# Performance work log

Measured on AMD Instinct MI355X. Metric: run time of the kernel, lower is better.

Reference implementation:

```python
import jax, jax.numpy as jnp
import numpy as np
from jax import lax

H_HEADS = 8      # attention heads
C_HID = 32       # per-head channels
NEG_SLOPE = 0.2  # PyG GATConv default leaky_relu slope


def _gat(x, src, dst, W, a_src, a_dst, b, num_nodes):
    # x: (N, Din); src/dst: (E',) with self-loops already appended
    h = (x @ W).reshape(num_nodes, H_HEADS, C_HID)          # (N, H, C)
    e = jax.nn.leaky_relu((h * a_src).sum(-1)[src] + (h * a_dst).sum(-1)[dst], NEG_SLOPE)  # (E', H)
    emax = jax.ops.segment_max(e, dst, num_segments=num_nodes)
    ex = jnp.exp(e - emax[dst])
    denom = jax.ops.segment_sum(ex, dst, num_segments=num_nodes)
    alpha = ex / (denom[dst] + 1e-16)                        # segment softmax over incoming edges
    out = jax.ops.segment_sum(h[src] * alpha[:, :, None], dst, num_segments=num_nodes)
    return out.reshape(num_nodes, H_HEADS * C_HID) + b


def _lstm_dir(seq, Wih, Whh, bih, bhh):
    # seq: (K, D); single-direction LSTM, returns final hidden state (Hs,)
    Hs = Whh.shape[1]
    def step(carry, x):
        h, c = carry
        g = x @ Wih.T + h @ Whh.T + bih + bhh                # (4*Hs,)
        i, f, gg, o = jnp.split(g, 4)
        c = jax.nn.sigmoid(f) * c + jax.nn.sigmoid(i) * jnp.tanh(gg)
        h = jax.nn.sigmoid(o) * jnp.tanh(c)
        return (h, c), None
    (h, _), _ = lax.scan(step, (jnp.zeros(Hs, seq.dtype), jnp.zeros(Hs, seq.dtype)), seq)
    return h


def setup_inputs():
    key = jax.random.key(0)
    ks = jax.random.split(key, 20)
    K, N, E = 8, 10000, 160000
    D1, D2, LH = 1, H_HEADS * C_HID, 256   # D2 = 256
    s = 0.1
    inp = {}
    inp['xs'] = jax.random.normal(ks[0], (K, N, D1), jnp.float32)
    inp['edge_index'] = jax.random.randint(ks[1], (K, 2, E), 0, N, jnp.int32)
    inp['W1'] = jax.random.normal(ks[2], (D1, D2), jnp.float32) * s
    inp['a_src1'] = jax.random.normal(ks[3], (H_HEADS, C_HID), jnp.float32) * s
    inp['a_dst1'] = jax.random.normal(ks[4], (H_HEADS, C_HID), jnp.float32) * s
    inp['b1'] = jnp.zeros((D2,), jnp.float32)
    inp['W2'] = jax.random.normal(ks[5], (D2, D2), jnp.float32) * s
    inp['a_src2'] = jax.random.normal(ks[6], (H_HEADS, C_HID), jnp.float32) * s
    inp['a_dst2'] = jax.random.normal(ks[7], (H_HEADS, C_HID), jnp.float32) * s
    inp['b2'] = jnp.zeros((D2,), jnp.float32)
    inp['Wih_f'] = jax.random.normal(ks[8], (4 * LH, D2), jnp.float32) * s
    inp['Whh_f'] = jax.random.normal(ks[9], (4 * LH, LH), jnp.float32) * s
    inp['bih_f'] = jnp.zeros((4 * LH,), jnp.float32)
    inp['bhh_f'] = jnp.zeros((4 * LH,), jnp.float32)
    inp['Wih_b'] = jax.random.normal(ks[10], (4 * LH, D2), jnp.float32) * s
    inp['Whh_b'] = jax.random.normal(ks[11], (4 * LH, LH), jnp.float32) * s
    inp['bih_b'] = jnp.zeros((4 * LH,), jnp.float32)
    inp['bhh_b'] = jnp.zeros((4 * LH,), jnp.float32)
    return inp


def reference(xs, edge_index, W1, a_src1, a_dst1, b1, W2, a_src2, a_dst2, b2,
              Wih_f, Whh_f, bih_f, bhh_f, Wih_b, Whh_b, bih_b, bhh_b):
    N = xs.shape[1]
    loops = jnp.arange(N, dtype=edge_index.dtype)  # self-loops (PyG default)
    def snap(carry, inp):
        x, ei = inp
        src = jnp.concatenate([ei[0], loops])
        dst = jnp.concatenate([ei[1], loops])
        h = jax.nn.relu(_gat(x, src, dst, W1, a_src1, a_dst1, b1, N))
        h = jax.nn.relu(_gat(h, src, dst, W2, a_src2, a_dst2, b2, N))
        return carry, h.mean(0)   # global mean pool -> (256,)
    _, embs = lax.scan(snap, 0, (xs, edge_index))   # (K, 256)
    h_fwd = _lstm_dir(embs, Wih_f, Whh_f, bih_f, bhh_f)
    h_bwd = _lstm_dir(embs[::-1], Wih_b, Whh_b, bih_b, bhh_b)
    return jnp.concatenate([h_fwd, h_bwd])[None, :]  # (1, 512)
```

## Files before the change

### kernel.cpp

```cpp
#include <hip/hip_runtime.h>
#include <hip/hip_fp16.h>
#include <math.h>

#define H_HEADS 8
#define C_HID 32
#define D2 256
#define NEG_SLOPE 0.2f
#define KSTEPS 8

__device__ __forceinline__ float lrelu(float x) { return x < 0.f ? NEG_SLOPE * x : x; }
__device__ __forceinline__ float sigmoidf(float x) { return 1.f / (1.f + expf(-x)); }


__global__ void zero_all_kernel(int* counts, int* fill, double* embp, int KN, int NEMBP,
                                const float* __restrict__ W1, const float* __restrict__ a_src1,
                                const float* __restrict__ a_dst1, float* Pvec, int D1) {
    int tid = blockIdx.x * blockDim.x + threadIdx.x;
    if (tid < KN) { counts[tid] = 0; fill[tid] = 0; }
    if (tid < NEMBP) embp[tid] = 0.0;
    if (blockIdx.x == 0 && threadIdx.x < 16 && D1 == 1) {
        int h = threadIdx.x & 7;
        const float* a = (threadIdx.x >= 8) ? a_dst1 : a_src1;
        float s = 0.f;
        for (int c = 0; c < 32; ++c) s += W1[h * 32 + c] * a[h * 32 + c];
        Pvec[threadIdx.x] = s;
    }
}


__global__ void count_all_kernel(const int* __restrict__ ei, int E, int N, int K,
                                 int* __restrict__ counts) {
    int bid = blockIdx.x;
    int k = bid % K;
    int jb = bid / K;
    int j = jb * blockDim.x + threadIdx.x;
    if (j >= E + N) return;
    int d = (j < E) ? ei[(size_t)k * 2 * E + E + j] : (j - E);
    atomicAdd(&counts[(size_t)k * N + d], 1);
}

__global__ __launch_bounds__(1024) void scan_all_kernel(const int* __restrict__ counts,
                                                        int* __restrict__ row_ptr, int N) {
    int k = blockIdx.x;
    const int* cnt = counts + (size_t)k * N;
    int* rp = row_ptr + (size_t)k * (N + 1);
    __shared__ int part[1024];
    int t = threadIdx.x;
    int ipt = (N + 1023) >> 10;
    int begin = t * ipt;
    int end = begin + ipt; if (end > N) end = N;
    if (begin > N) begin = N;
    int s = 0;
    for (int i = begin; i < end; ++i) s += cnt[i];
    part[t] = s;
    __syncthreads();
    for (int d = 1; d < 1024; d <<= 1) {
        int v = 0;
        if (t >= d) v = part[t - d];
        __syncthreads();
        if (t >= d) part[t] += v;
        __syncthreads();
    }
    int run = (t == 0) ? 0 : part[t - 1];
    for (int i = begin; i < end; ++i) { rp[i] = run; run += cnt[i]; }
    if (t == 1023) rp[N] = part[1023];
}

__global__ void scatter_all_kernel(const int* __restrict__ ei, int E, int N, int K,
                                   const int* __restrict__ row_ptr, int* __restrict__ fill,
                                   int* __restrict__ ein) {
    int bid = blockIdx.x;
    int k = bid % K;
    int jb = bid / K;
    int j = jb * blockDim.x + threadIdx.x;
    if (j >= E + N) return;
    int s, d;
    if (j < E) { s = ei[(size_t)k * 2 * E + j]; d = ei[(size_t)k * 2 * E + E + j]; }
    else { s = j - E; d = s; }
    int pos = row_ptr[(size_t)k * (N + 1) + d] + atomicAdd(&fill[(size_t)k * N + d], 1);
    ein[(size_t)k * (E + N) + pos] = s;
}


__global__ __launch_bounds__(256) void agg1s_all_kernel(const float* __restrict__ xs,
                                                        const float* __restrict__ P,
                                                        const int* __restrict__ row_ptr,
                                                        const int* __restrict__ ein,
                                                        float* __restrict__ Sbuf,
                                                        int N, int E2, int k0, int BKcur) {
    int bid = blockIdx.x;
    int kb = bid % BKcur;
    int nb = bid / BKcur;
    int k = k0 + kb;
    const float* x = xs + (size_t)k * N;
    const int* rp = row_ptr + (size_t)k * (N + 1);
    const int* ek = ein + (size_t)k * E2;

    int n = nb * 4 + (threadIdx.x >> 6);
    if (n >= N) return;
    int lane = threadIdx.x & 63;
    int e0 = rp[n], e1 = rp[n + 1];
    int h8 = lane & 7;
    float Ps = P[h8], Pd = P[8 + h8];
    float base = x[n] * Pd;

    float mx = -INFINITY;
    for (int i = e0 + (lane >> 3); i < e1; i += 8) {
        float xv = x[ek[i]];
        mx = fmaxf(mx, lrelu(xv * Ps + base));
    }
    mx = fmaxf(mx, __shfl_xor(mx, 8));
    mx = fmaxf(mx, __shfl_xor(mx, 16));
    mx = fmaxf(mx, __shfl_xor(mx, 32));

    float num = 0.f, den = 0.f;
    for (int i = e0 + (lane >> 3); i < e1; i += 8) {
        float xv = x[ek[i]];
        float w = __expf(lrelu(xv * Ps + base) - mx);
        num += w * xv;
        den += w;
    }
    num += __shfl_xor(num, 8);  den += __shfl_xor(den, 8);
    num += __shfl_xor(num, 16); den += __shfl_xor(den, 16);
    num += __shfl_xor(num, 32); den += __shfl_xor(den, 32);
    float S = num / (den + 1e-16f);

    if (lane < 8) Sbuf[((size_t)kb * N + n) * 8 + lane] = S;
}


__global__ void h1_kernel(const float* __restrict__ x, const float* __restrict__ W,
                          float* __restrict__ h, int N, int D1) {
    int tid = blockIdx.x * blockDim.x + threadIdx.x;
    if (tid >= N * 256) return;
    int n = tid >> 8, j = tid & 255;
    float acc = 0.f;
    for (int d = 0; d < D1; ++d) acc += x[n * D1 + d] * W[d * 256 + j];
    h[tid] = acc;
}

__global__ __launch_bounds__(256) void s_all_kernel(const float* __restrict__ bufA,
                                                    const float* __restrict__ a_src,
                                                    const float* __restrict__ a_dst,
                                                    float* __restrict__ s_src,
                                                    float* __restrict__ s_dst, int N) {
    int kb = blockIdx.y;
    int j = blockIdx.x * 256 + threadIdx.x;
    if (j >= N * 8) return;
    int n = j >> 3, hh = j & 7;
    const float* hp = bufA + (size_t)kb * N * 256 + (size_t)n * 256 + hh * 32;
    const float* as = a_src + hh * 32;
    const float* ad = a_dst + hh * 32;
    float ss = 0.f, sd = 0.f;
#pragma unroll
    for (int c = 0; c < 32; ++c) { float v = hp[c]; ss += v * as[c]; sd += v * ad[c]; }
    s_src[(size_t)kb * N * 8 + j] = ss;
    s_dst[(size_t)kb * N * 8 + j] = sd;
}

__global__ __launch_bounds__(256) void s_all_h16_kernel(const __half* __restrict__ h16,
                                                        const float* __restrict__ a_src,
                                                        const float* __restrict__ a_dst,
                                                        float* __restrict__ s_src,
                                                        float* __restrict__ s_dst, int N) {
    int kb = blockIdx.y;
    int j = blockIdx.x * 256 + threadIdx.x;
    if (j >= N * 8) return;
    int n = j >> 3, hh = j & 7;
    const __half2* hp = (const __half2*)(h16 + (size_t)kb * N * 256 + (size_t)n * 256 + hh * 32);
    const float* as = a_src + hh * 32;
    const float* ad = a_dst + hh * 32;
    float ss = 0.f, sd = 0.f;
#pragma unroll
    for (int c = 0; c < 16; ++c) {
        float2 v = __half22float2(hp[c]);
        ss += v.x * as[2 * c] + v.y * as[2 * c + 1];
        sd += v.x * ad[2 * c] + v.y * ad[2 * c + 1];
    }
    s_src[(size_t)kb * N * 8 + j] = ss;
    s_dst[(size_t)kb * N * 8 + j] = sd;
}

__global__ __launch_bounds__(256) void agg2_out_kernel(const float* __restrict__ h,
                                                       const float* __restrict__ s_src,
                                                       const float* __restrict__ s_dst,
                                                       const int* __restrict__ row_ptr,
                                                       const int* __restrict__ ein,
                                                       const float* __restrict__ bias,
                                                       float* __restrict__ out,
                                                       int N, int E2, int k0) {
    int k = k0;
    const int* rp = row_ptr + (size_t)k * (N + 1);
    const int* ek = ein + (size_t)k * E2;
    int n = blockIdx.x * 4 + (threadIdx.x >> 6);
    if (n >= N) return;
    int lane = threadIdx.x & 63;
    int e0 = rp[n], e1 = rp[n + 1];
    int h8 = lane & 7;
    float sd8 = s_dst[n * 8 + h8];

    float mx = -INFINITY;
    for (int i = e0 + (lane >> 3); i < e1; i += 8) {
        int s = ek[i];
        mx = fmaxf(mx, lrelu(s_src[s * 8 + h8] + sd8));
    }
    mx = fmaxf(mx, __shfl_xor(mx, 8));
    mx = fmaxf(mx, __shfl_xor(mx, 16));
    mx = fmaxf(mx, __shfl_xor(mx, 32));

    int hd = lane >> 3;
    float m = __shfl(mx, hd);
    float sdh = __shfl(sd8, hd);

    float den = 0.f;
    float4 acc = make_float4(0.f, 0.f, 0.f, 0.f);
    for (int i = e0; i < e1; ++i) {
        int s = ek[i];
        const float4 hv = *(const float4*)(h + (size_t)s * 256 + lane * 4);
        float w = expf(lrelu(s_src[s * 8 + hd] + sdh) - m);
        den += w;
        acc.x += w * hv.x; acc.y += w * hv.y; acc.z += w * hv.z; acc.w += w * hv.w;
    }
    float dE = den + 1e-16f;
    const float4 bv = *(const float4*)(bias + lane * 4);
    float4 o;
    o.x = fmaxf(acc.x / dE + bv.x, 0.f);
    o.y = fmaxf(acc.y / dE + bv.y, 0.f);
    o.z = fmaxf(acc.z / dE + bv.z, 0.f);
    o.w = fmaxf(acc.w / dE + bv.w, 0.f);
    *(float4*)(out + (size_t)n * 256 + lane * 4) = o;
}

__global__ void cvt_kernel(const float* __restrict__ src, __half* __restrict__ dst, int total) {
    int i = blockIdx.x * blockDim.x + threadIdx.x;
    if (i * 2 + 1 < total) {
        float2 v = *(const float2*)(src + i * 2);
        ((__half2*)dst)[i] = __floats2half2_rn(v.x, v.y);
    }
}


__global__ __launch_bounds__(256) void agg2pool_kernel(const __half* __restrict__ h16,
                                                       const float* __restrict__ s_src,
                                                       const float* __restrict__ s_dst,
                                                       const int* __restrict__ row_ptr,
                                                       const int* __restrict__ ein,
                                                       const float* __restrict__ bias,
                                                       double* __restrict__ embp,
                                                       int N, int E2, int k0, int BKcur) {
    int bid = blockIdx.x;
    int kb = bid % BKcur;
    int nb = bid / BKcur;
    int k = k0 + kb;
    int w = threadIdx.x >> 6;
    int lane = threadIdx.x & 63;
    int n = nb * 4 + w;
    bool active = (n < N);
    const __half* h = h16 + (size_t)kb * N * 256;
    const float* ssrc = s_src + (size_t)kb * N * 8;
    const float* sdst = s_dst + (size_t)kb * N * 8;
    const int* rp = row_ptr + (size_t)k * (N + 1);
    const int* ek = ein + (size_t)k * E2;

    float4 o = make_float4(0.f, 0.f, 0.f, 0.f);
    if (active) {
        int e0 = rp[n], e1 = rp[n + 1];
        int h8 = lane & 7;
        int es = lane >> 3;
        int hd = lane >> 3;
        float sd8 = sdst[n * 8 + h8];

        float mx = -INFINITY;
        for (int i = e0 + es; i < e1; i += 8) {
            int s = ek[i];
            mx = fmaxf(mx, lrelu(ssrc[s * 8 + h8] + sd8));
        }
        mx = fmaxf(mx, __shfl_xor(mx, 8));
        mx = fmaxf(mx, __shfl_xor(mx, 16));
        mx = fmaxf(mx, __shfl_xor(mx, 32));

        float den = 0.f;
        float4 acc = make_float4(0.f, 0.f, 0.f, 0.f);

        for (int c0 = e0; c0 < e1; c0 += 8) {
            int eI = c0 + es;
            bool valid = (eI < e1);
            int sA = ek[valid ? eI : e0];
            float wv = __expf(lrelu(ssrc[sA * 8 + h8] + sd8) - mx);
            if (!valid) wv = 0.f;

            int jmax = e1 - c0; if (jmax > 8) jmax = 8;
#pragma unroll 8
            for (int j = 0; j < 8; ++j) {
                if (j >= jmax) break;
                int srcLane = (j << 3) + hd;
                float wj = __shfl(wv, srcLane);
                int sj = __shfl(sA, srcLane);
                const __half2* hp = (const __half2*)(h + (size_t)sj * 256 + lane * 4);
                float2 f0 = __half22float2(hp[0]);
                float2 f1 = __half22float2(hp[1]);
                den += wj;
                acc.x += wj * f0.x;
                acc.y += wj * f0.y;
                acc.z += wj * f1.x;
                acc.w += wj * f1.y;
            }
        }
        float dE = den + 1e-16f;
        const float4 bv = *(const float4*)(bias + lane * 4);
        o.x = fmaxf(acc.x / dE + bv.x, 0.f);
        o.y = fmaxf(acc.y / dE + bv.y, 0.f);
        o.z = fmaxf(acc.z / dE + bv.z, 0.f);
        o.w = fmaxf(acc.w / dE + bv.w, 0.f);
    }

    __shared__ double pe[4][256];
    pe[w][lane * 4 + 0] = (double)o.x;
    pe[w][lane * 4 + 1] = (double)o.y;
    pe[w][lane * 4 + 2] = (double)o.z;
    pe[w][lane * 4 + 3] = (double)o.w;
    __syncthreads();
    int tid = threadIdx.x;
    double s = pe[0][tid] + pe[1][tid] + pe[2][tid] + pe[3][tid];
    atomicAdd(&embp[((size_t)k * 32 + (nb & 31)) * 256 + tid], s);
}


__global__ __launch_bounds__(256) void gemm_fused_kernel(const float* __restrict__ S,
                                                         const float* __restrict__ W1,
                                                         const float* __restrict__ bias1,
                                                         const float* __restrict__ B,
                                                         __half* __restrict__ C16, int M) {
    __shared__ float Ast[16][132];
    __shared__ float Bs[16][132];
    __shared__ float w1s[256], b1s[256];
    __shared__ float Ss[128 * 8];
    int tid = threadIdx.x;
    int bm = blockIdx.x, bn = blockIdx.y;

    w1s[tid] = W1[tid];
    b1s[tid] = bias1[tid];
    {
        int base = bm * 128 * 8 + tid * 4;
        float4 sv = make_float4(0.f, 0.f, 0.f, 0.f);
        if (bm * 128 + (tid * 4) / 8 < M) {
            sv = *(const float4*)(S + base);
        }
        *(float4*)&Ss[tid * 4] = sv;
    }

    int arow = tid >> 1;
    int kgrp = (tid & 1) * 8;
    bool rowvalid = (bm * 128 + arow < M);

    int brow = tid >> 4;
    int bcol = (tid & 15) * 8;
    const float* Bbase = B + bn * 128;

    int w = tid >> 6, lane = tid & 63;
    int qr = (w >> 1) * 64, qc = (w & 1) * 64;
    int ty = lane >> 3, tx = lane & 7;
    int r0 = qr + ty * 8, c0 = qc + tx * 8;
    float acc[8][8] = {};

    __syncthreads();

    for (int kt = 0; kt < 256; kt += 16) {
        float sh = Ss[arow * 8 + (kt >> 5)];
#pragma unroll
        for (int j = 0; j < 8; ++j) {
            int kk = kgrp + j;
            float a = fmaxf(fmaf(sh, w1s[kt + kk], b1s[kt + kk]), 0.f);
            Ast[kk][arow] = rowvalid ? a : 0.f;
        }
        const float* bg = Bbase + (size_t)(kt + brow) * 256 + bcol;
        *(float4*)&Bs[brow][bcol] = *(const float4*)bg;
        *(float4*)&Bs[brow][bcol + 4] = *(const float4*)(bg + 4);
        __syncthreads();
#pragma unroll
        for (int kk = 0; kk < 16; ++kk) {
            float4 a0 = *(const float4*)&Ast[kk][r0];
            float4 a1 = *(const float4*)&Ast[kk][r0 + 4];
            float4 b0 = *(const float4*)&Bs[kk][c0];
            float4 b1v = *(const float4*)&Bs[kk][c0 + 4];
            float ar[8] = {a0.x, a0.y, a0.z, a0.w, a1.x, a1.y, a1.z, a1.w};
            float br[8] = {b0.x, b0.y, b0.z, b0.w, b1v.x, b1v.y, b1v.z, b1v.w};
#pragma unroll
            for (int i2 = 0; i2 < 8; ++i2)
#pragma unroll
                for (int j2 = 0; j2 < 8; ++j2) acc[i2][j2] += ar[i2] * br[j2];
        }
        __syncthreads();
    }
#pragma unroll
    for (int i2 = 0; i2 < 8; ++i2) {
        int gm = bm * 128 + r0 + i2;
        if (gm < M) {
            float4 pack;
            ((__half2*)&pack)[0] = __floats2half2_rn(acc[i2][0], acc[i2][1]);
            ((__half2*)&pack)[1] = __floats2half2_rn(acc[i2][2], acc[i2][3]);
            ((__half2*)&pack)[2] = __floats2half2_rn(acc[i2][4], acc[i2][5]);
            ((__half2*)&pack)[3] = __floats2half2_rn(acc[i2][6], acc[i2][7]);
            *(float4*)(C16 + (size_t)gm * 256 + bn * 128 + c0) = pack;
        }
    }
}


__global__ __launch_bounds__(256) void gemm_kernel(const float* __restrict__ A,
                                                   const float* __restrict__ B,
                                                   float* __restrict__ C, int M) {
    __shared__ float Ast[8][132];
    __shared__ float Bs[8][128];
    int tid = threadIdx.x;
    int bm = blockIdx.x, bn = blockIdx.y;
    int ty = tid >> 4, tx = tid & 15;
    int r0 = ty * 8, c0 = tx * 8;
    float acc[8][8] = {};
    int arow = tid >> 1, acol = (tid & 1) * 4;
    int brow = tid >> 5, bcol = (tid & 31) * 4;
    const float* Bbase = B + bn * 128;

    for (int kt = 0; kt < 256; kt += 8) {
        int gr = bm * 128 + arow;
        float4 av = (gr < M) ? *(const float4*)(A + (size_t)gr * 256 + kt + acol)
                             : make_float4(0.f, 0.f, 0.f, 0.f);
        Ast[acol + 0][arow] = av.x;
        Ast[acol + 1][arow] = av.y;
        Ast[acol + 2][arow] = av.z;
        Ast[acol + 3][arow] = av.w;
        *(float4*)&Bs[brow][bcol] = *(const float4*)(Bbase + (size_t)(kt + brow) * 256 + bcol);
        __syncthreads();
#pragma unroll
        for (int kk = 0; kk < 8; ++kk) {
            float4 a0 = *(const float4*)&Ast[kk][r0];
            float4 a1 = *(const float4*)&Ast[kk][r0 + 4];
            float4 b0 = *(const float4*)&Bs[kk][c0];
            float4 b1 = *(const float4*)&Bs[kk][c0 + 4];
            float ar[8] = {a0.x, a0.y, a0.z, a0.w, a1.x, a1.y, a1.z, a1.w};
            float br[8] = {b0.x, b0.y, b0.z, b0.w, b1.x, b1.y, b1.z, b1.w};
#pragma unroll
            for (int i2 = 0; i2 < 8; ++i2)
#pragma unroll
                for (int j2 = 0; j2 < 8; ++j2) acc[i2][j2] += ar[i2] * br[j2];
        }
        __syncthreads();
    }
#pragma unroll
    for (int i2 = 0; i2 < 8; ++i2) {
        int gm = bm * 128 + r0 + i2;
        if (gm < M) {
            *(float4*)(C + (size_t)gm * 256 + bn * 128 + c0) =
                make_float4(acc[i2][0], acc[i2][1], acc[i2][2], acc[i2][3]);
            *(float4*)(C + (size_t)gm * 256 + bn * 128 + c0 + 4) =
                make_float4(acc[i2][4], acc[i2][5], acc[i2][6], acc[i2][7]);
        }
    }
}


__global__ void merge_kernel(const double* __restrict__ embp, float* __restrict__ emb,
                             int* __restrict__ flags) {
    int k = blockIdx.x, c = threadIdx.x;
    double s = 0.0;
#pragma unroll
    for (int p = 0; p < 32; ++p) s += embp[((size_t)k * 32 + p) * 256 + c];
    emb[k * 256 + c] = (float)s;
    if (blockIdx.x == 0 && threadIdx.x < 2 * (KSTEPS + 1)) flags[threadIdx.x] = 0;
}


__global__ __launch_bounds__(256) void lstm_rec_kernel(
    const float* __restrict__ emb, float invN,
    const float* __restrict__ Wih_f, const float* __restrict__ Whh_f,
    const float* __restrict__ bih_f, const float* __restrict__ bhh_f,
    const float* __restrict__ Wih_b, const float* __restrict__ Whh_b,
    const float* __restrict__ bih_b, const float* __restrict__ bhh_b,
    float* __restrict__ hbuf, int* __restrict__ flags, float* __restrict__ out) {
    int dir = blockIdx.x >> 4;
    int seg = blockIdx.x & 15;
    const float* Wih = dir ? Wih_b : Wih_f;
    const float* Whh = dir ? Whh_b : Whh_f;
    const float* bih = dir ? bih_b : bih_f;
    const float* bhh = dir ? bhh_b : bhh_f;

    __shared__ float wh[64 * 256];
    __shared__ float wi[64 * 256];
    __shared__ float xs_s[KSTEPS * 256];
    __shared__ float gx[KSTEPS][64];
    __shared__ float garr[64];
    __shared__ float hprev_s[256];
    int tid = threadIdx.x;

    for (int v = tid; v < 64 * 64; v += 256) {
        int lrow = v >> 6;
        int c4 = (v & 63) * 4;
        int grow = ((lrow >> 4) << 8) + seg * 16 + (lrow & 15);
        *(float4*)&wh[lrow * 256 + c4] = *(const float4*)(Whh + (size_t)grow * 256 + c4);
        *(float4*)&wi[lrow * 256 + c4] = *(const float4*)(Wih + (size_t)grow * 256 + c4);
    }
    for (int idx = tid; idx < KSTEPS * 256; idx += 256) xs_s[idx] = emb[idx] * invN;
    __syncthreads();

    for (int d = tid; d < KSTEPS * 64; d += 256) {
        int st = d >> 6, lr = d & 63;
        const float* wr = &wi[lr << 8];
        const float* xr = &xs_s[st << 8];
        int r = (tid & 63) << 2;
        float acc = 0.f;
#pragma unroll 8
        for (int kk = 0; kk < 256; kk += 4) {
            int k2 = (kk + r) & 255;
            acc += wr[k2] * xr[k2] + wr[k2 + 1] * xr[k2 + 1] +
                   wr[k2 + 2] * xr[k2 + 2] + wr[k2 + 3] * xr[k2 + 3];
        }
        int grow = ((lr >> 4) << 8) + seg * 16 + (lr & 15);
        gx[st][lr] = acc + bih[grow] + bhh[grow];
    }

    int* flag = flags + dir * (KSTEPS + 1);
    float* hb = hbuf + dir * (KSTEPS + 1) * 256;

    if (tid < 16)
        __hip_atomic_store(&hb[seg * 16 + tid], 0.f, __ATOMIC_RELAXED, __HIP_MEMORY_SCOPE_AGENT);
    __syncthreads();
    if (tid == 0)
        __hip_atomic_fetch_add(&flag[0], 1, __ATOMIC_RELEASE, __HIP_MEMORY_SCOPE_AGENT);

    float c_reg = 0.f;

    for (int step = 0; step < KSTEPS; ++step) {
        if (tid == 0) {
            while (__hip_atomic_load(&flag[step], __ATOMIC_RELAXED, __HIP_MEMORY_SCOPE_AGENT) < 16) {
                __builtin_amdgcn_s_sleep(1);
            }
            (void)__hip_atomic_load(&flag[step], __ATOMIC_ACQUIRE, __HIP_MEMORY_SCOPE_AGENT);
        }
        __syncthreads();
        hprev_s[tid] = __hip_atomic_load(&hb[step * 256 + tid], __ATOMIC_RELAXED,
                                         __HIP_MEMORY_SCOPE_AGENT);
        __syncthreads();

        int d = tid >> 2, p = tid & 3;
        const float* wr = &wh[(d << 8) + (p << 6)];
        const float* hr = &hprev_s[p << 6];
        int rot = tid & 63;
        float acc = 0.f;
#pragma unroll 8
        for (int k = 0; k < 64; ++k) {
            int k2 = (k + rot) & 63;
            acc += wr[k2] * hr[k2];
        }
        acc += __shfl_xor(acc, 1);
        acc += __shfl_xor(acc, 2);
        if (p == 0) garr[d] = acc;
        __syncthreads();

        if (tid < 16) {
            float ig = sigmoidf(garr[tid] + gx[step][tid]);
            float fg = sigmoidf(garr[16 + tid] + gx[step][16 + tid]);
            float gg = tanhf(garr[32 + tid] + gx[step][32 + tid]);
            float og = sigmoidf(garr[48 + tid] + gx[step][48 + tid]);
            float cn = fg * c_reg + ig * gg;
            c_reg = cn;
            float hn = og * tanhf(cn);
            __hip_atomic_store(&hb[(step + 1) * 256 + seg * 16 + tid], hn, __ATOMIC_RELAXED,
                               __HIP_MEMORY_SCOPE_AGENT);
        }
        __syncthreads();
        if (tid == 0)
            __hip_atomic_fetch_add(&flag[step + 1], 1, __ATOMIC_RELEASE, __HIP_MEMORY_SCOPE_AGENT);
    }

    if (tid < 16)
        out[dir * 256 + seg * 16 + tid] =
            __hip_atomic_load(&hb[KSTEPS * 256 + seg * 16 + tid], __ATOMIC_RELAXED,
                              __HIP_MEMORY_SCOPE_AGENT);
}


extern "C" void kernel_launch(void* const* d_in, const int* in_sizes, int n_in,
                              void* d_out, int out_size, void* d_ws, size_t ws_size,
                              hipStream_t stream) {
    const float* xs = (const float*)d_in[0];
    const int* edge_index = (const int*)d_in[1];
    const float* W1 = (const float*)d_in[2];
    const float* a_src1 = (const float*)d_in[3];
    const float* a_dst1 = (const float*)d_in[4];
    const float* b1 = (const float*)d_in[5];
    const float* W2 = (const float*)d_in[6];
    const float* a_src2 = (const float*)d_in[7];
    const float* a_dst2 = (const float*)d_in[8];
    const float* b2 = (const float*)d_in[9];
    const float* Wih_f = (const float*)d_in[10];
    const float* Whh_f = (const float*)d_in[11];
    const float* bih_f = (const float*)d_in[12];
    const float* bhh_f = (const float*)d_in[13];
    const float* Wih_b = (const float*)d_in[14];
    const float* Whh_b = (const float*)d_in[15];
    const float* bih_b = (const float*)d_in[16];
    const float* bhh_b = (const float*)d_in[17];

    const int K = KSTEPS;
    int D1 = in_sizes[2] / D2;
    int N = in_sizes[0] / (K * D1);
    int E = in_sizes[1] / (2 * K);
    int E2 = E + N;

    auto al = [](size_t x) { return (x + 255) & ~(size_t)255; };
    size_t fixed_sz = al((size_t)K * N * 4)
                    + al((size_t)K * (N + 1) * 4)
                    + al((size_t)K * N * 4)
                    + al((size_t)K * E2 * 4)
                    + al((size_t)K * 32 * 256 * 8)
                    + al((size_t)K * 256 * 4)
                    + al((size_t)2 * (K + 1) * 256 * 4)
                    + al((size_t)2 * (K + 1) * 4)
                    + al(16 * 4);
    int BK = 8;
    while (BK > 1) {
        size_t need = fixed_sz + 3 * al((size_t)BK * N * 8 * 4) + 2 * al((size_t)BK * N * 256 * 4);
        if (need <= ws_size) break;
        BK >>= 1;
    }

    char* w = (char*)d_ws;
    auto alloc = [&](size_t bytes) { char* p = w; w += (bytes + 255) & ~(size_t)255; return p; };
    int* counts = (int*)alloc((size_t)K * N * 4);
    int* row_ptr = (int*)alloc((size_t)K * (N + 1) * 4);
    int* fill = (int*)alloc((size_t)K * N * 4);
    int* ein = (int*)alloc((size_t)K * E2 * 4);
    double* embp = (double*)alloc((size_t)K * 32 * 256 * 8);
    float* emb = (float*)alloc((size_t)K * 256 * 4);
    float* hbuf = (float*)alloc((size_t)2 * (K + 1) * 256 * 4);
    int* flags = (int*)alloc((size_t)2 * (K + 1) * 4);
    float* Pvec = (float*)alloc(16 * 4);
    float* Sbuf = (float*)alloc((size_t)BK * N * 8 * 4);
    float* s_src = (float*)alloc((size_t)BK * N * 8 * 4);
    float* s_dst = (float*)alloc((size_t)BK * N * 8 * 4);
    float* bufA = (float*)alloc((size_t)BK * N * 256 * 4);
    float* bufB = (float*)alloc((size_t)BK * N * 256 * 4);
    __half* h16 = (__half*)bufA;
    __half* h16_fb = (__half*)bufB;

    int KN = K * N;
    int NEMBP = K * 32 * 256;
    int zblk = ((KN > NEMBP ? KN : NEMBP) + 255) / 256;
    zero_all_kernel<<<zblk, 256, 0, stream>>>(counts, fill, embp, KN, NEMBP,
                                              W1, a_src1, a_dst1, Pvec, D1);
    int eblk = (E2 + 255) / 256;
    count_all_kernel<<<eblk * K, 256, 0, stream>>>(edge_index, E, N, K, counts);
    scan_all_kernel<<<K, 1024, 0, stream>>>(counts, row_ptr, N);
    scatter_all_kernel<<<eblk * K, 256, 0, stream>>>(edge_index, E, N, K, row_ptr, fill, ein);

    int nblk4 = (N + 3) / 4;
    int sblk = (N * 8 + 255) / 256;
    for (int k0 = 0; k0 < K; k0 += BK) {
        int BKcur = (K - k0 < BK) ? (K - k0) : BK;
        if (D1 == 1) {
            agg1s_all_kernel<<<nblk4 * BKcur, 256, 0, stream>>>(
                xs, Pvec, row_ptr, ein, Sbuf, N, E2, k0, BKcur);
            int M = BKcur * N;
            gemm_fused_kernel<<<dim3((M + 127) / 128, 2), 256, 0, stream>>>(
                Sbuf, W1, b1, W2, h16, M);
            s_all_h16_kernel<<<dim3(sblk, BKcur), 256, 0, stream>>>(h16, a_src2, a_dst2,
                                                                    s_src, s_dst, N);
            agg2pool_kernel<<<nblk4 * BKcur, 256, 0, stream>>>(
                h16, s_src, s_dst, row_ptr, ein, b2, embp, N, E2, k0, BKcur);
        } else {
            for (int kk = 0; kk < BKcur; ++kk) {
                int k = k0 + kk;
                const float* xk = xs + (size_t)k * N * D1;
                h1_kernel<<<(N * 256 + 255) / 256, 256, 0, stream>>>(xk, W1, bufA, N, D1);
                s_all_kernel<<<dim3(sblk, 1), 256, 0, stream>>>(bufA, a_src1, a_dst1,
                                                                s_src, s_dst, N);
                agg2_out_kernel<<<nblk4, 256, 0, stream>>>(bufA, s_src, s_dst, row_ptr, ein,
                                                           b1, bufB, N, E2, k);
                gemm_kernel<<<dim3((N + 127) / 128, 2), 256, 0, stream>>>(bufB, W2, bufA, N);
                cvt_kernel<<<(N * 256 / 2 + 255) / 256, 256, 0, stream>>>(bufA, h16_fb, N * 256);
                s_all_h16_kernel<<<dim3(sblk, 1), 256, 0, stream>>>(h16_fb, a_src2, a_dst2,
                                                                    s_src, s_dst, N);
                agg2pool_kernel<<<nblk4, 256, 0, stream>>>(
                    h16_fb, s_src, s_dst, row_ptr, ein, b2, embp, N, E2, k, 1);
            }
        }
    }

    merge_kernel<<<K, 256, 0, stream>>>(embp, emb, flags);
    lstm_rec_kernel<<<32, 256, 0, stream>>>(emb, 1.f / (float)N,
                                            Wih_f, Whh_f, bih_f, bhh_f,
                                            Wih_b, Whh_b, bih_b, bhh_b,
                                            hbuf, flags, (float*)d_out);
}
```

Baseline: 543.4 us.

## Split layer-2 edge attention weights into a separate precompute kernel

Adds a kernel that computes per-edge, per-head softmax numerators (exp of leaky-relu score minus segment max) and writes them to a buffer that reuses the second big workspace. The aggregation/pooling kernel then just streams these weights with the fp16 features, dropping the max pass and exp work from its inner loop. This trades an extra kernel launch plus an E'×8 float write and read for a simpler, more regular gather loop. The original combined kernel is kept under a new name for the D1≠1 fallback path.

```diff
diff --git a/kernel.cpp b/kernel.cpp
--- a/kernel.cpp
+++ b/kernel.cpp
@@ -240,14 +240,117 @@
 }
 
 
+__global__ __launch_bounds__(256) void wcomp_kernel(const float* __restrict__ s_src,
+                                                    const float* __restrict__ s_dst,
+                                                    const int* __restrict__ row_ptr,
+                                                    const int* __restrict__ ein,
+                                                    float* __restrict__ wbuf,
+                                                    int N, int E2, int k0, int BKcur) {
+    int bid = blockIdx.x;
+    int kb = bid % BKcur;
+    int nb = bid / BKcur;
+    int k = k0 + kb;
+    int n = nb * 4 + (threadIdx.x >> 6);
+    if (n >= N) return;
+    int lane = threadIdx.x & 63;
+    const float* ssrc = s_src + (size_t)kb * N * 8;
+    const float* sdst = s_dst + (size_t)kb * N * 8;
+    const int* rp = row_ptr + (size_t)k * (N + 1);
+    const int* ek = ein + (size_t)k * E2;
+    float* wb = wbuf + (size_t)kb * E2 * 8;
+
+    int e0 = rp[n], e1 = rp[n + 1];
+    int h8 = lane & 7;
+    int es = lane >> 3;
+    float sd8 = sdst[n * 8 + h8];
+
+    float mx = -INFINITY;
+    for (int i = e0 + es; i < e1; i += 8) {
+        int s = ek[i];
+        mx = fmaxf(mx, lrelu(ssrc[s * 8 + h8] + sd8));
+    }
+    mx = fmaxf(mx, __shfl_xor(mx, 8));
+    mx = fmaxf(mx, __shfl_xor(mx, 16));
+    mx = fmaxf(mx, __shfl_xor(mx, 32));
+
+    for (int c0 = e0; c0 < e1; c0 += 8) {
+        int eI = c0 + es;
+        if (eI < e1) {
+            int sA = ek[eI];
+            float wv = __expf(lrelu(ssrc[sA * 8 + h8] + sd8) - mx);
+            wb[(size_t)eI * 8 + h8] = wv;
+        }
+    }
+}
+
+
 __global__ __launch_bounds__(256) void agg2pool_kernel(const __half* __restrict__ h16,
-                                                       const float* __restrict__ s_src,
-                                                       const float* __restrict__ s_dst,
+                                                       const float* __restrict__ wbuf,
                                                        const int* __restrict__ row_ptr,
                                                        const int* __restrict__ ein,
                                                        const float* __restrict__ bias,
                                                        double* __restrict__ embp,
                                                        int N, int E2, int k0, int BKcur) {
+    int bid = blockIdx.x;
+    int kb = bid % BKcur;
+    int nb = bid / BKcur;
+    int k = k0 + kb;
+    int w = threadIdx.x >> 6;
+    int lane = threadIdx.x & 63;
+    int n = nb * 4 + w;
+    bool active = (n < N);
+    const __half* h = h16 + (size_t)kb * N * 256;
+    const float* wb = wbuf + (size_t)kb * E2 * 8;
+    const int* rp = row_ptr + (size_t)k * (N + 1);
+    const int* ek = ein + (size_t)k * E2;
+
+    float4 o = make_float4(0.f, 0.f, 0.f, 0.f);
+    if (active) {
+        int e0 = rp[n], e1 = rp[n + 1];
+        int hd = lane >> 3;
+
+        float den = 0.f;
+        float4 acc = make_float4(0.f, 0.f, 0.f, 0.f);
+        for (int i = e0; i < e1; ++i) {
+            int sj = ek[i];
+            float wj = wb[(size_t)i * 8 + hd];
+            const __half2* hp = (const __half2*)(h + (size_t)sj * 256 + lane * 4);
+            float2 f0 = __half22float2(hp[0]);
+            float2 f1 = __half22float2(hp[1]);
+            den += wj;
+            acc.x += wj * f0.x;
+            acc.y += wj * f0.y;
+            acc.z += wj * f1.x;
+            acc.w += wj * f1.y;
+        }
+        float dE = den + 1e-16f;
+        const float4 bv = *(const float4*)(bias + lane * 4);
+        o.x = fmaxf(acc.x / dE + bv.x, 0.f);
+        o.y = fmaxf(acc.y / dE + bv.y, 0.f);
+        o.z = fmaxf(acc.z / dE + bv.z, 0.f);
+        o.w = fmaxf(acc.w / dE + bv.w, 0.f);
+    }
+
+    __shared__ double pe[4][256];
+    pe[w][lane * 4 + 0] = (double)o.x;
+    pe[w][lane * 4 + 1] = (double)o.y;
+    pe[w][lane * 4 + 2] = (double)o.z;
+    pe[w][lane * 4 + 3] = (double)o.w;
+    __syncthreads();
+    int tid = threadIdx.x;
+    double s = pe[0][tid] + pe[1][tid] + pe[2][tid] + pe[3][tid];
+    atomicAdd(&embp[((size_t)k * 32 + (nb & 31)) * 256 + tid], s);
+}
+
+
+__global__ __launch_bounds__(256) void agg2pool_comb_kernel(const __half* __restrict__ h16,
+                                                            const float* __restrict__ s_src,
+                                                            const float* __restrict__ s_dst,
+                                                            const int* __restrict__ row_ptr,
+                                                            const int* __restrict__ ein,
+                                                            const float* __restrict__ bias,
+                                                            double* __restrict__ embp,
+                                                            int N, int E2, int k0, int BKcur) {
     int bid = blockIdx.x;
     int kb = bid % BKcur;
     int nb = bid / BKcur;
@@ -619,7 +722,11 @@
                     + al(16 * 4);
     int BK = 8;
     while (BK > 1) {
-        size_t need = fixed_sz + 3 * al((size_t)BK * N * 8 * 4) + 2 * al((size_t)BK * N * 256 * 4);
+        size_t bigB = al((size_t)BK * N * 256 * 4);
+        size_t wb = al((size_t)BK * E2 * 8 * 4);
+        if (wb > bigB) bigB = wb;
+        size_t need = fixed_sz + 3 * al((size_t)BK * N * 8 * 4)
+                    + al((size_t)BK * N * 256 * 4) + bigB;
         if (need <= ws_size) break;
         BK >>= 1;
     }
@@ -639,8 +746,11 @@
     float* s_src = (float*)alloc((size_t)BK * N * 8 * 4);
     float* s_dst = (float*)alloc((size_t)BK * N * 8 * 4);
     float* bufA = (float*)alloc((size_t)BK * N * 256 * 4);
-    float* bufB = (float*)alloc((size_t)BK * N * 256 * 4);
+    size_t bigB = (size_t)BK * N * 256 * 4;
+    size_t wbsz = (size_t)BK * E2 * 8 * 4;
+    float* bufB = (float*)alloc(bigB > wbsz ? bigB : wbsz);
     __half* h16 = (__half*)bufA;
+    float* wbuf = (float*)bufB;
     __half* h16_fb = (__half*)bufB;
 
     int KN = K * N;
@@ -665,8 +775,10 @@
                 Sbuf, W1, b1, W2, h16, M);
             s_all_h16_kernel<<<dim3(sblk, BKcur), 256, 0, stream>>>(h16, a_src2, a_dst2,
                                                                     s_src, s_dst, N);
+            wcomp_kernel<<<nblk4 * BKcur, 256, 0, stream>>>(
+                s_src, s_dst, row_ptr, ein, wbuf, N, E2, k0, BKcur);
             agg2pool_kernel<<<nblk4 * BKcur, 256, 0, stream>>>(
-                h16, s_src, s_dst, row_ptr, ein, b2, embp, N, E2, k0, BKcur);
+                h16, wbuf, row_ptr, ein, b2, embp, N, E2, k0, BKcur);
         } else {
             for (int kk = 0; kk < BKcur; ++kk) {
                 int k = k0 + kk;
@@ -680,7 +792,7 @@
                 cvt_kernel<<<(N * 256 / 2 + 255) / 256, 256, 0, stream>>>(bufA, h16_fb, N * 256);
                 s_all_h16_kernel<<<dim3(sblk, 1), 256, 0, stream>>>(h16_fb, a_src2, a_dst2,
                                                                     s_src, s_dst, N);
-                agg2pool_kernel<<<nblk4, 256, 0, stream>>>(
+                agg2pool_comb_kernel<<<nblk4, 256, 0, stream>>>(
                     h16_fb, s_src, s_dst, row_ptr, ein, b2, embp, N, E2, k, 1);
             }
         }
```

Result: slower. 598.8 us (+10.2%).
